# Performance work log

Measured on AMD Instinct MI355X. Metric: run time of the kernel, lower is better.

Reference implementation:

```python
import jax, jax.numpy as jnp
from jax import lax
import numpy as np

INPUT_SIZE = 256
HIDDEN = 256


def _gru_scan(x, W_ih, W_hh, b_ih, b_hh):
    # x: [b, t, in], PyTorch GRU gate order: r, z, n
    b, t, _ = x.shape
    k = W_hh.shape[1]
    # precompute input contribution for all timesteps: [b, t, 3k]
    gx = jnp.einsum('bti,gi->btg', x, W_ih) + b_ih

    def step(h, gxt):
        gh = h @ W_hh.T + b_hh                 # [b, 3k]
        xr, xz, xn = jnp.split(gxt, 3, axis=-1)
        hr, hz, hn = jnp.split(gh, 3, axis=-1)
        r = jax.nn.sigmoid(xr + hr)
        z = jax.nn.sigmoid(xz + hz)
        n = jnp.tanh(xn + r * hn)
        h_new = (1.0 - z) * n + z * h
        return h_new, h_new

    h0 = jnp.zeros((b, k), x.dtype)
    _, hs = lax.scan(step, h0, jnp.swapaxes(gx, 0, 1))  # hs: [t, b, k]
    return hs


def setup_inputs() -> dict:
    key = jax.random.key(0)
    kx, k1, k2, k3, k4 = jax.random.split(key, 5)
    s_ih = 1.0 / np.sqrt(HIDDEN)
    x = jax.random.normal(kx, (32, 2048, INPUT_SIZE), dtype=jnp.float32)
    W_ih = jax.random.uniform(k1, (3 * HIDDEN, INPUT_SIZE), jnp.float32, -s_ih, s_ih)
    W_hh = jax.random.uniform(k2, (3 * HIDDEN, HIDDEN), jnp.float32, -s_ih, s_ih)
    b_ih = jax.random.uniform(k3, (3 * HIDDEN,), jnp.float32, -s_ih, s_ih)
    b_hh = jax.random.uniform(k4, (3 * HIDDEN,), jnp.float32, -s_ih, s_ih)
    return {'x': x, 'W_ih': W_ih, 'W_hh': W_hh, 'b_ih': b_ih, 'b_hh': b_hh}


def reference(x, W_ih, W_hh, b_ih, b_hh):
    # forward direction
    hs_f = _gru_scan(x, W_ih, W_hh, b_ih, b_hh)                     # [t, b, k]
    # 'bidirectional': same weights applied to time-reversed input
    hs_r = _gru_scan(x[:, ::-1, :], W_ih, W_hh, b_ih, b_hh)[::-1]   # [t, b, k]
    outputs = jnp.concatenate(
        (jnp.swapaxes(hs_f, 0, 1), jnp.swapaxes(hs_r, 0, 1)), axis=2)  # [b, t, 2k]
    hiddens = jnp.concatenate((hs_f, hs_r), axis=2)                    # [t, b, 2k]
    return outputs, hiddens
```

## Files before the change

### kernel.cpp

```cpp
#include <hip/hip_runtime.h>
#include <hip/hip_fp16.h>


typedef __fp16 half2_t __attribute__((ext_vector_type(2)));

static constexpr int T_STEPS = 2048;
static constexpr int BATCH   = 32;
static constexpr int HID     = 256;
static constexpr int IN      = 256;
static constexpr int G3      = 768;

__device__ __forceinline__ float fdot2(half2_t a, half2_t b, float c) {
#if __has_builtin(__builtin_amdgcn_fdot2)
    return __builtin_amdgcn_fdot2(a, b, c, false);
#else
    return c + (float)a[0] * (float)b[0] + (float)a[1] * (float)b[1];
#endif
}

__global__ __launch_bounds__(256, 2) void gx_gemm(
        const float* __restrict__ x,
        const float* __restrict__ Wih,
        const float* __restrict__ bih,
        _Float16* __restrict__ gx) {
    __shared__ ushort As[64 * 256];
    __shared__ ushort Bs[64 * 256];

    const int tid = threadIdx.x;
    const int m0  = blockIdx.x * 64;
    const int tx  = tid & 15;
    const int ty  = tid >> 4;

#pragma unroll
    for (int i = 0; i < 16; ++i) {
        int f    = tid + 256 * i;
        int row  = f >> 6;
        int col4 = f & 63;
        float4 v = *(const float4*)(x + (size_t)(m0 + row) * IN + col4 * 4);
        half2_t h0 = __builtin_amdgcn_cvt_pkrtz(v.x, v.y);
        half2_t h1 = __builtin_amdgcn_cvt_pkrtz(v.z, v.w);
        int chunk = col4 >> 1;
        int idx = row * 256 + ((chunk ^ (row & 7)) * 8) + (col4 & 1) * 4;
        uint2 wv;
        wv.x = __builtin_bit_cast(unsigned, h0);
        wv.y = __builtin_bit_cast(unsigned, h1);
        *(uint2*)(As + idx) = wv;
    }

    for (int nb = 0; nb < 12; ++nb) {
#pragma unroll
        for (int i = 0; i < 16; ++i) {
            int f    = tid + 256 * i;
            int row  = f >> 6;
            int col4 = f & 63;
            float4 v = *(const float4*)(Wih + (size_t)(nb * 64 + row) * IN + col4 * 4);
            half2_t h0 = __builtin_amdgcn_cvt_pkrtz(v.x, v.y);
            half2_t h1 = __builtin_amdgcn_cvt_pkrtz(v.z, v.w);
            int chunk = col4 >> 1;
            int idx = row * 256 + ((chunk ^ (row & 7)) * 8) + (col4 & 1) * 4;
            uint2 wv;
            wv.x = __builtin_bit_cast(unsigned, h0);
            wv.y = __builtin_bit_cast(unsigned, h1);
            *(uint2*)(Bs + idx) = wv;
        }
        __syncthreads();

        float acc[4][4];
#pragma unroll
        for (int jm = 0; jm < 4; ++jm)
#pragma unroll
            for (int jn = 0; jn < 4; ++jn) acc[jm][jn] = 0.f;

#pragma unroll 4
        for (int kc = 0; kc < 32; ++kc) {
            union { uint4 u; half2_t h[4]; } av[4], bv[4];
#pragma unroll
            for (int jm = 0; jm < 4; ++jm) {
                int r = ty * 4 + jm;
                av[jm].u = *(const uint4*)(As + r * 256 + ((kc ^ (r & 7)) * 8));
            }
#pragma unroll
            for (int jn = 0; jn < 4; ++jn) {
                int r = tx + 16 * jn;
                bv[jn].u = *(const uint4*)(Bs + r * 256 + ((kc ^ (r & 7)) * 8));
            }
#pragma unroll
            for (int jm = 0; jm < 4; ++jm)
#pragma unroll
                for (int jn = 0; jn < 4; ++jn)
#pragma unroll
                    for (int p = 0; p < 4; ++p)
                        acc[jm][jn] = fdot2(av[jm].h[p], bv[jn].h[p], acc[jm][jn]);
        }

#pragma unroll
        for (int jn = 0; jn < 4; ++jn) {
            int n = nb * 64 + tx + 16 * jn;
            float bias = bih[n];
#pragma unroll
            for (int jm = 0; jm < 4; ++jm) {
                int m = m0 + ty * 4 + jm;
                gx[(size_t)m * G3 + n] = (_Float16)(acc[jm][jn] + bias);
            }
        }
        __syncthreads();
    }
}

__global__ __launch_bounds__(512, 2) void gru_seq(
        const _Float16* __restrict__ gx,
        const float* __restrict__ Whh,
        const float* __restrict__ bhh,
        float* __restrict__ out0,
        float* __restrict__ out1) {
    __shared__ float  P[4 * 768];
    __shared__ ushort h16[256];
    __shared__ ushort gxb[768];

    const int tid = threadIdx.x;
    const int b   = blockIdx.x & 31;
    const int d   = blockIdx.x >> 5;
    const int w   = tid >> 6;
    const int L   = tid & 63;
    const int s   = w & 3;
    const int g   = w >> 2;

    half2_t Wr[6][32];
#pragma unroll
    for (int jr = 0; jr < 6; ++jr) {
        const float* wrow = Whh + (size_t)(g * 384 + jr * 64 + L) * HID + s * 64;
#pragma unroll
        for (int q = 0; q < 32; ++q) {
            float2 wv = *(const float2*)(wrow + 2 * q);
            Wr[jr][q] = __builtin_amdgcn_cvt_pkrtz(wv.x, wv.y);
        }
    }

    float bh_r = 0.f, bh_z = 0.f, bh_n = 0.f, hprev = 0.f;
    if (tid < 256) {
        bh_r = bhh[tid];
        bh_z = bhh[256 + tid];
        bh_n = bhh[512 + tid];
        h16[tid] = 0;
    }
    __syncthreads();

    const size_t gxbase = (size_t)b * T_STEPS * G3;

    for (int t = 0; t < T_STEPS; ++t) {
        const int tp = d ? (T_STEPS - 1 - t) : t;

        uint4 gxv;
        if (tid < 96)
            gxv = *(const uint4*)(gx + gxbase + (size_t)tp * G3 + tid * 8);

        float acc[6] = {0.f, 0.f, 0.f, 0.f, 0.f, 0.f};
#pragma unroll
        for (int c = 0; c < 4; ++c) {
            union { uint4 u; half2_t h[4]; } hh0, hh1;
            hh0.u = *(const uint4*)(h16 + s * 64 + c * 16);
            hh1.u = *(const uint4*)(h16 + s * 64 + c * 16 + 8);
#pragma unroll
            for (int jr = 0; jr < 6; ++jr) {
#pragma unroll
                for (int p = 0; p < 4; ++p) {
                    acc[jr] = fdot2(Wr[jr][c * 8 + p],     hh0.h[p], acc[jr]);
                    acc[jr] = fdot2(Wr[jr][c * 8 + 4 + p], hh1.h[p], acc[jr]);
                }
            }
        }
#pragma unroll
        for (int jr = 0; jr < 6; ++jr)
            P[s * 768 + g * 384 + jr * 64 + L] = acc[jr];

        if (tid < 96)
            *(uint4*)(gxb + tid * 8) = gxv;

        __syncthreads();

        if (tid < 256) {
            const int i = tid;
            float hr = P[i]       + P[768 + i]       + P[1536 + i]       + P[2304 + i];
            float hz = P[256 + i] + P[768 + 256 + i] + P[1536 + 256 + i] + P[2304 + 256 + i];
            float hn = P[512 + i] + P[768 + 512 + i] + P[1536 + 512 + i] + P[2304 + 512 + i];
            const _Float16* gxh = (const _Float16*)gxb;
            float gr = (float)gxh[i];
            float gz = (float)gxh[256 + i];
            float gn = (float)gxh[512 + i];

            float r = 1.f / (1.f + __expf(-(gr + hr + bh_r)));
            float z = 1.f / (1.f + __expf(-(gz + hz + bh_z)));
            float nx = gn + r * (hn + bh_n);
            nx = fminf(fmaxf(nx, -15.f), 15.f);
            float e = __expf(2.f * nx);
            float n = (e - 1.f) / (e + 1.f);
            float h = n + z * (hprev - n);
            hprev = h;

            h16[i] = __builtin_bit_cast(ushort, (_Float16)h);
            out0[((size_t)b * T_STEPS + tp) * 512 + d * 256 + i] = h;
            out1[((size_t)tp * BATCH + b) * 512 + d * 256 + i]   = h;
        }
        __syncthreads();
    }
}

extern "C" void kernel_launch(void* const* d_in, const int* in_sizes, int n_in,
                              void* d_out, int out_size, void* d_ws, size_t ws_size,
                              hipStream_t stream) {
    const float* x   = (const float*)d_in[0];
    const float* Wih = (const float*)d_in[1];
    const float* Whh = (const float*)d_in[2];
    const float* bih = (const float*)d_in[3];
    const float* bhh = (const float*)d_in[4];

    float* out0 = (float*)d_out;
    float* out1 = out0 + (size_t)BATCH * T_STEPS * 512;

    _Float16* gx = (_Float16*)d_ws;

    gx_gemm<<<dim3(65536 / 64), dim3(256), 0, stream>>>(x, Wih, bih, gx);
    gru_seq<<<dim3(BATCH * 2), dim3(512), 0, stream>>>(gx, Whh, bhh, out0, out1);
}
```

Measured before the change: 2.621 ms.

## Spread GRU recurrence across 768 threads with prefetch, fast math and lighter barriers

The sequential GRU kernel now runs 12 waves instead of 8. Each thread holds 4 weight rows rather than 6, the recurrent bias is folded into the accumulator, and the next timestep's gx vector is prefetched into registers one step ahead. The gate math moves to hardware exp2/rcp intrinsics without clamping, output pointers are advanced incrementally, and __syncthreads is replaced by an lgkmcnt-only wait plus s_barrier. These aim to shorten the per-step critical path, at the cost of relying on the barrier only ordering LDS and of possible overflow edge cases in the tanh formula.

```diff
diff --git a/kernel.cpp b/kernel.cpp
--- a/kernel.cpp
+++ b/kernel.cpp
@@ -11,11 +11,11 @@
 static constexpr int G3      = 768;
 
 __device__ __forceinline__ float fdot2(half2_t a, half2_t b, float c) {
-#if __has_builtin(__builtin_amdgcn_fdot2)
     return __builtin_amdgcn_fdot2(a, b, c, false);
-#else
-    return c + (float)a[0] * (float)b[0] + (float)a[1] * (float)b[1];
-#endif
+}
+
+__device__ __forceinline__ void barrier_lgkm() {
+    asm volatile("s_waitcnt lgkmcnt(0)\n\ts_barrier" ::: "memory");
 }
 
 __global__ __launch_bounds__(256, 2) void gx_gemm(
@@ -56,14 +56,14 @@
             float4 v = *(const float4*)(Wih + (size_t)(nb * 64 + row) * IN + col4 * 4);
             half2_t h0 = __builtin_amdgcn_cvt_pkrtz(v.x, v.y);
             half2_t h1 = __builtin_amdgcn_cvt_pkrtz(v.z, v.w);
-            int chunk = col4 >> 1;
+        int chunk = col4 >> 1;
             int idx = row * 256 + ((chunk ^ (row & 7)) * 8) + (col4 & 1) * 4;
             uint2 wv;
             wv.x = __builtin_bit_cast(unsigned, h0);
             wv.y = __builtin_bit_cast(unsigned, h1);
             *(uint2*)(Bs + idx) = wv;
         }
-        __syncthreads();
+        barrier_lgkm();
 
         float acc[4][4];
 #pragma unroll
@@ -103,11 +103,11 @@
                 gx[(size_t)m * G3 + n] = (_Float16)(acc[jm][jn] + bias);
             }
         }
-        __syncthreads();
-    }
-}
-
-__global__ __launch_bounds__(512, 2) void gru_seq(
+        barrier_lgkm();
+    }
+}
+
+__global__ __launch_bounds__(768, 3) void gru_seq(
         const _Float16* __restrict__ gx,
         const float* __restrict__ Whh,
         const float* __restrict__ bhh,
@@ -125,43 +125,55 @@
     const int s   = w & 3;
     const int g   = w >> 2;
 
-    half2_t Wr[6][32];
-#pragma unroll
-    for (int jr = 0; jr < 6; ++jr) {
-        const float* wrow = Whh + (size_t)(g * 384 + jr * 64 + L) * HID + s * 64;
+    half2_t Wr[4][32];
+    float   Wb[4];
+#pragma unroll
+    for (int jr = 0; jr < 4; ++jr) {
+        const int row = g * 256 + jr * 64 + L;
+        const float* wrow = Whh + (size_t)row * HID + s * 64;
 #pragma unroll
         for (int q = 0; q < 32; ++q) {
             float2 wv = *(const float2*)(wrow + 2 * q);
             Wr[jr][q] = __builtin_amdgcn_cvt_pkrtz(wv.x, wv.y);
         }
-    }
-
-    float bh_r = 0.f, bh_z = 0.f, bh_n = 0.f, hprev = 0.f;
-    if (tid < 256) {
-        bh_r = bhh[tid];
-        bh_z = bhh[256 + tid];
-        bh_n = bhh[512 + tid];
-        h16[tid] = 0;
-    }
+        Wb[jr] = (s == 0) ? bhh[row] : 0.f;
+    }
+
+    float hprev = 0.f;
+    if (tid < 256) h16[tid] = 0;
+
+    const int tp0 = d ? (T_STEPS - 1) : 0;
+    const int sgn = d ? -1 : 1;
+
+    const _Float16* gp = gx + ((size_t)b * T_STEPS + tp0) * G3 + tid * 8;
+    const int gpd = sgn * G3;
+    uint4 greg{};
+    if (tid < 96) greg = *(const uint4*)gp;
+
+    float* o0 = out0 + ((size_t)b * T_STEPS + tp0) * 512 + d * 256 + tid;
+    float* o1 = out1 + ((size_t)tp0 * BATCH + b) * 512 + d * 256 + tid;
+    const int o0d = sgn * 512;
+    const int o1d = sgn * (BATCH * 512);
+
     __syncthreads();
 
-    const size_t gxbase = (size_t)b * T_STEPS * G3;
-
     for (int t = 0; t < T_STEPS; ++t) {
-        const int tp = d ? (T_STEPS - 1 - t) : t;
-
-        uint4 gxv;
-        if (tid < 96)
-            gxv = *(const uint4*)(gx + gxbase + (size_t)tp * G3 + tid * 8);
-
-        float acc[6] = {0.f, 0.f, 0.f, 0.f, 0.f, 0.f};
+        if (tid < 96) {
+            *(uint4*)(gxb + tid * 8) = greg;
+            if (t + 1 < T_STEPS) {
+                gp += gpd;
+                greg = *(const uint4*)gp;
+            }
+        }
+
+        float acc[4] = {Wb[0], Wb[1], Wb[2], Wb[3]};
 #pragma unroll
         for (int c = 0; c < 4; ++c) {
             union { uint4 u; half2_t h[4]; } hh0, hh1;
             hh0.u = *(const uint4*)(h16 + s * 64 + c * 16);
             hh1.u = *(const uint4*)(h16 + s * 64 + c * 16 + 8);
 #pragma unroll
-            for (int jr = 0; jr < 6; ++jr) {
+            for (int jr = 0; jr < 4; ++jr) {
 #pragma unroll
                 for (int p = 0; p < 4; ++p) {
                     acc[jr] = fdot2(Wr[jr][c * 8 + p],     hh0.h[p], acc[jr]);
@@ -170,38 +182,32 @@
             }
         }
 #pragma unroll
-        for (int jr = 0; jr < 6; ++jr)
-            P[s * 768 + g * 384 + jr * 64 + L] = acc[jr];
-
-        if (tid < 96)
-            *(uint4*)(gxb + tid * 8) = gxv;
-
-        __syncthreads();
+        for (int jr = 0; jr < 4; ++jr)
+            P[s * 768 + g * 256 + jr * 64 + L] = acc[jr];
+
+        barrier_lgkm();
 
         if (tid < 256) {
             const int i = tid;
-            float hr = P[i]       + P[768 + i]       + P[1536 + i]       + P[2304 + i];
-            float hz = P[256 + i] + P[768 + 256 + i] + P[1536 + 256 + i] + P[2304 + 256 + i];
-            float hn = P[512 + i] + P[768 + 512 + i] + P[1536 + 512 + i] + P[2304 + 512 + i];
+            float hr = (P[i]       + P[768 + i])  + (P[1536 + i] + P[2304 + i]);
+            float hz = (P[256 + i] + P[1024 + i]) + (P[1792 + i] + P[2560 + i]);
+            float hn = (P[512 + i] + P[1280 + i]) + (P[2048 + i] + P[2816 + i]);
             const _Float16* gxh = (const _Float16*)gxb;
-            float gr = (float)gxh[i];
-            float gz = (float)gxh[256 + i];
-            float gn = (float)gxh[512 + i];
-
-            float r = 1.f / (1.f + __expf(-(gr + hr + bh_r)));
-            float z = 1.f / (1.f + __expf(-(gz + hz + bh_z)));
-            float nx = gn + r * (hn + bh_n);
-            nx = fminf(fmaxf(nx, -15.f), 15.f);
-            float e = __expf(2.f * nx);
-            float n = (e - 1.f) / (e + 1.f);
-            float h = n + z * (hprev - n);
+            float xr = (float)gxh[i]       + hr;
+            float xz = (float)gxh[256 + i] + hz;
+            float r = __builtin_amdgcn_rcpf(1.f + __builtin_amdgcn_exp2f(xr * -1.44269504f));
+            float z = __builtin_amdgcn_rcpf(1.f + __builtin_amdgcn_exp2f(xz * -1.44269504f));
+            float nx = (float)gxh[512 + i] + r * hn;
+            float e2 = __builtin_amdgcn_exp2f(nx * 2.88539008f);
+            float n  = 1.f - 2.f * __builtin_amdgcn_rcpf(1.f + e2);
+            float h  = n + z * (hprev - n);
             hprev = h;
 
             h16[i] = __builtin_bit_cast(ushort, (_Float16)h);
-            out0[((size_t)b * T_STEPS + tp) * 512 + d * 256 + i] = h;
-            out1[((size_t)tp * BATCH + b) * 512 + d * 256 + i]   = h;
-        }
-        __syncthreads();
+            *o0 = h; *o1 = h;
+            o0 += o0d; o1 += o1d;
+        }
+        barrier_lgkm();
     }
 }
 
@@ -220,5 +226,5 @@
     _Float16* gx = (_Float16*)d_ws;
 
     gx_gemm<<<dim3(65536 / 64), dim3(256), 0, stream>>>(x, Wih, bih, gx);
-    gru_seq<<<dim3(BATCH * 2), dim3(512), 0, stream>>>(gx, Whh, bhh, out0, out1);
-}
+    gru_seq<<<dim3(BATCH * 2), dim3(768), 0, stream>>>(gx, Whh, bhh, out0, out1);
+}
```

New measurement: 2.565 ms. 2.1% less time.
